# Performance work log

Measured on AMD Instinct MI355X. Metric: run time of the kernel, lower is better.

The kernel has to match this reference:

```python
import jax, jax.numpy as jnp
import numpy as np

# Emformer config (from torchaudio.models.Emformer in BasicNet4)
D, H, FFN, L = 512, 4, 128, 4      # input_dim, num_heads, ffn_dim, num_layers
SEG, RC = 4, 1                     # segment_length, right_context_length
B, T = 8, 1025
U = T - RC                         # utterance length = 1024
NSEG = -(-U // SEG)                # 256 segments
R = NSEG * RC                      # total right-context frames = 256
DH = D // H


def _right_context_indices():
    # torchaudio _gen_right_context: segment i's right context = frames [(i+1)*SEG : (i+1)*SEG+RC],
    # last block = input[T-RC:]
    idx = [np.arange((i + 1) * SEG, (i + 1) * SEG + RC) for i in range(NSEG - 1)]
    idx.append(np.arange(T - RC, T))
    return np.concatenate(idx)


def _attention_mask():
    # Rows / cols ordered [right-context blocks (seg order), utterance frames].
    # A query belonging to segment i may attend to segment i's right-context block
    # and segment i's utterance frames (left_context_length=0, no memory bank).
    seg_rc = np.repeat(np.arange(NSEG), RC)
    seg_u = np.arange(U) // SEG
    seg_q = np.concatenate([seg_rc, seg_u])
    seg_k = np.concatenate([seg_rc, seg_u])
    return seg_q[:, None] == seg_k[None, :]  # (R+U, R+U), True = allowed


def _ln(x, g, b, eps=1e-5):
    mu = jnp.mean(x, -1, keepdims=True)
    var = jnp.mean(jnp.square(x - mu), -1, keepdims=True)
    return (x - mu) * jax.lax.rsqrt(var + eps) * g + b


def setup_inputs() -> dict:
    key = jax.random.key(0)
    ks = jax.random.split(key, 8)
    s = 0.02
    return {
        "x": jax.random.normal(ks[0], (B, T, D), jnp.float32),
        "Wq": jax.random.normal(ks[1], (L, D, D), jnp.float32) * s,
        "bq": jnp.zeros((L, D), jnp.float32),
        "Wkv": jax.random.normal(ks[2], (L, 2 * D, D), jnp.float32) * s,
        "bkv": jnp.zeros((L, 2 * D), jnp.float32),
        "Wo": jax.random.normal(ks[3], (L, D, D), jnp.float32) * s,
        "bo": jnp.zeros((L, D), jnp.float32),
        "W1": jax.random.normal(ks[4], (L, FFN, D), jnp.float32) * s,
        "b1": jnp.zeros((L, FFN), jnp.float32),
        "W2": jax.random.normal(ks[5], (L, D, FFN), jnp.float32) * s,
        "b2": jnp.zeros((L, D), jnp.float32),
        "ln_in_g": jnp.ones((L, D), jnp.float32),
        "ln_in_b": jnp.zeros((L, D), jnp.float32),
        "ff_ln_g": jnp.ones((L, D), jnp.float32),
        "ff_ln_b": jnp.zeros((L, D), jnp.float32),
        "ln_out_g": jnp.ones((L, D), jnp.float32),
        "ln_out_b": jnp.zeros((L, D), jnp.float32),
    }


def reference(x, Wq, bq, Wkv, bkv, Wo, bo, W1, b1, W2, b2,
              ln_in_g, ln_in_b, ff_ln_g, ff_ln_b, ln_out_g, ln_out_b):
    rc_idx = jnp.asarray(_right_context_indices())
    allowed = jnp.asarray(_attention_mask())
    scale = DH ** -0.5
    u = x[:, :U]          # (B, U, D) utterance
    r = x[:, rc_idx]      # (B, R, D) gathered right-context blocks
    for l in range(L):
        cat = jnp.concatenate([r, u], axis=1)            # (B, R+U, D)
        ln = _ln(cat, ln_in_g[l], ln_in_b[l])            # pre-attention LN
        q = (ln @ Wq[l].T + bq[l]).reshape(B, R + U, H, DH)
        kv = ln @ Wkv[l].T + bkv[l]
        k = kv[..., :D].reshape(B, R + U, H, DH)
        v = kv[..., D:].reshape(B, R + U, H, DH)
        scores = jnp.einsum("bqhd,bkhd->bhqk", q * scale, k)
        scores = jnp.where(allowed, scores, -jnp.inf)
        probs = jax.nn.softmax(scores, axis=-1)
        attn = jnp.einsum("bhqk,bkhd->bqhd", probs, v).reshape(B, R + U, D)
        rc_out = attn @ Wo[l].T + bo[l] + cat            # residual w/ pre-LN input
        h = _ln(rc_out, ff_ln_g[l], ff_ln_b[l])
        h = jax.nn.relu(h @ W1[l].T + b1[l]) @ W2[l].T + b2[l]
        rc_out = _ln(rc_out + h, ln_out_g[l], ln_out_b[l])
        r, u = rc_out[:, :R], rc_out[:, R:]
    return u.mean(axis=1)  # (B, D): mean-pool over utterance frames
```

## Files before the change

### kernel.cpp

```cpp
#include <hip/hip_runtime.h>
#include <cstdint>
#include <cstddef>

#define D_    512
#define H_    4
#define DH_   128
#define FFN_  128
#define L_    4
#define B_    8
#define T_    1025
#define U_    1024
#define NSEG_ 256
#define R_    256
#define TOT_  1280
#define M_    (B_*TOT_)
#define CH_   1536

typedef __attribute__((ext_vector_type(8))) short bf16x8;
typedef __attribute__((ext_vector_type(4))) float f32x4;
typedef unsigned short u16;

__device__ __forceinline__ u16 f2bf(float f) {
  unsigned u = __builtin_bit_cast(unsigned, f);
  u += 0x7fff + ((u >> 16) & 1);
  return (u16)(u >> 16);
}
__device__ __forceinline__ float bf2f(u16 h) {
  unsigned u = ((unsigned)h) << 16;
  return __builtin_bit_cast(float, u);
}

__device__ __forceinline__ void gload_lds16(const void* g, void* l) {
  __builtin_amdgcn_global_load_lds(
      (const __attribute__((address_space(1))) unsigned*)g,
      (__attribute__((address_space(3))) unsigned*)l, 16, 0, 0);
}

__global__ __launch_bounds__(256)
void cvt_all_k(const float* __restrict__ Wq, const float* __restrict__ Wkv,
               const float* __restrict__ Wo, const float* __restrict__ W1,
               const float* __restrict__ W2, const float* __restrict__ bq,
               const float* __restrict__ bkv,
               u16* __restrict__ WQKVb, u16* __restrict__ Wob,
               u16* __restrict__ W1b, u16* __restrict__ W2b,
               float* __restrict__ bQKV) {
  int i4 = blockIdx.x * 256 + threadIdx.x;
  if (i4 < 786432) {
    int e = i4 * 4;
    int l = e / 786432;
    int rem = e - l * 786432;
    int n = rem >> 9, k = rem & 511;
    const float* src = (n < 512) ? (Wq + (size_t)l * 262144 + n * 512 + k)
                                 : (Wkv + (size_t)l * 524288 + (n - 512) * 512 + k);
    float4 v = *(const float4*)src;
    ushort4 o; o.x = f2bf(v.x); o.y = f2bf(v.y); o.z = f2bf(v.z); o.w = f2bf(v.w);
    *(ushort4*)(WQKVb + e) = o;
  } else if (i4 < 1048576) {
    int e = (i4 - 786432) * 4;
    float4 v = *(const float4*)(Wo + e);
    ushort4 o; o.x = f2bf(v.x); o.y = f2bf(v.y); o.z = f2bf(v.z); o.w = f2bf(v.w);
    *(ushort4*)(Wob + e) = o;
  } else if (i4 < 1114112) {
    int e = (i4 - 1048576) * 4;
    float4 v = *(const float4*)(W1 + e);
    ushort4 o; o.x = f2bf(v.x); o.y = f2bf(v.y); o.z = f2bf(v.z); o.w = f2bf(v.w);
    *(ushort4*)(W1b + e) = o;
  } else if (i4 < 1179648) {
    int e = (i4 - 1114112) * 4;
    float4 v = *(const float4*)(W2 + e);
    ushort4 o; o.x = f2bf(v.x); o.y = f2bf(v.y); o.z = f2bf(v.z); o.w = f2bf(v.w);
    *(ushort4*)(W2b + e) = o;
  } else if (i4 < 1181184) {
    int e = (i4 - 1179648) * 4;
    int l = e / 1536, n = e - l * 1536;
#pragma unroll
    for (int t = 0; t < 4; ++t) {
      int nn = n + t;
      bQKV[e + t] = (nn < 512) ? bq[l * 512 + nn] : bkv[l * 1024 + (nn - 512)];
    }
  }
}

__global__ __launch_bounds__(256)
void gather_ln_k(const float* __restrict__ x, const float* __restrict__ g,
                 const float* __restrict__ bb, float* __restrict__ X,
                 u16* __restrict__ LNb) {
  int row = blockIdx.x;
  int tid = threadIdx.x;
  int b = row / TOT_, p = row % TOT_;
  int t = (p < R_) ? ((p < R_ - 1) ? 4 * (p + 1) : (T_ - 1)) : (p - R_);
  const float* xr = x + ((size_t)b * T_ + t) * D_;
  float e0 = xr[tid], e1 = xr[tid + 256];
  X[(size_t)row * D_ + tid] = e0;
  X[(size_t)row * D_ + tid + 256] = e1;
  float s = e0 + e1, ss = e0 * e0 + e1 * e1;
#pragma unroll
  for (int off = 32; off > 0; off >>= 1) {
    s  += __shfl_down(s, off);
    ss += __shfl_down(ss, off);
  }
  __shared__ float red[10];
  int wid = tid >> 6, lane = tid & 63;
  if (lane == 0) { red[wid] = s; red[4 + wid] = ss; }
  __syncthreads();
  if (tid == 0) {
    float S = red[0] + red[1] + red[2] + red[3];
    float SS = red[4] + red[5] + red[6] + red[7];
    float mu = S * (1.0f / D_);
    float var = SS * (1.0f / D_) - mu * mu;
    if (var < 0.f) var = 0.f;
    red[8] = mu; red[9] = rsqrtf(var + 1e-5f);
  }
  __syncthreads();
  float mu = red[8], rs = red[9];
  u16* yr = LNb + (size_t)row * D_;
  yr[tid]       = f2bf((e0 - mu) * rs * g[tid]       + bb[tid]);
  yr[tid + 256] = f2bf((e1 - mu) * rs * g[tid + 256] + bb[tid + 256]);
}

#define GBK 32

__global__ __launch_bounds__(256)
void gemm_qkv(const u16* __restrict__ A, const u16* __restrict__ Bw,
              const float* __restrict__ bias, u16* __restrict__ Cout) {
  __shared__ __align__(16) u16 As[128 * GBK];
  __shared__ __align__(16) u16 Bs[128 * GBK];
  const int tid = threadIdx.x;
  const int wid = tid >> 6;
  const int lane = tid & 63;
  const int bid = blockIdx.x;
  const int xcd = bid & 7;
  const int t = bid >> 3;
  const int cb = t % 12;
  const int rb = xcd * 10 + t / 12;
  const int bm = rb * 128;
  const int bn = cb * 128;
  const int wr = wid >> 1, wc = wid & 1;

  const int srow = tid >> 2;
  const int skoff = (tid & 3) << 3;

  f32x4 acc[4][4] = {};

  const u16* Ag0 = A  + (size_t)(bm + srow)      * D_ + skoff;
  const u16* Ag1 = A  + (size_t)(bm + 64 + srow) * D_ + skoff;
  const u16* Bg0 = Bw + (size_t)(bn + srow)      * D_ + skoff;
  const u16* Bg1 = Bw + (size_t)(bn + 64 + srow) * D_ + skoff;
  u16* AsW0 = &As[(size_t)(wid * 16)      * GBK];
  u16* AsW1 = &As[(size_t)(64 + wid * 16) * GBK];
  u16* BsW0 = &Bs[(size_t)(wid * 16)      * GBK];
  u16* BsW1 = &Bs[(size_t)(64 + wid * 16) * GBK];

  const int lrow = lane & 15;
  const int lko  = (lane >> 4) * 16;

  for (int k0 = 0; k0 < D_; k0 += GBK) {
    __syncthreads();
    gload_lds16(Ag0 + k0, AsW0);
    gload_lds16(Ag1 + k0, AsW1);
    gload_lds16(Bg0 + k0, BsW0);
    gload_lds16(Bg1 + k0, BsW1);
    __syncthreads();

    bf16x8 afrag[4], bfrag[4];
#pragma unroll
    for (int m = 0; m < 4; ++m) {
      int row = wr * 64 + m * 16 + lrow;
      afrag[m] = *(const bf16x8*)((const char*)As + row * (GBK * 2) + lko);
    }
#pragma unroll
    for (int n = 0; n < 4; ++n) {
      int col = wc * 64 + n * 16 + lrow;
      bfrag[n] = *(const bf16x8*)((const char*)Bs + col * (GBK * 2) + lko);
    }
#pragma unroll
    for (int m = 0; m < 4; ++m)
#pragma unroll
      for (int n = 0; n < 4; ++n)
        acc[m][n] = __builtin_amdgcn_mfma_f32_16x16x32_bf16(
            afrag[m], bfrag[n], acc[m][n], 0, 0, 0);
  }

  const int lcol  = lane & 15;
  const int lrow4 = (lane >> 4) * 4;
#pragma unroll
  for (int m = 0; m < 4; ++m) {
    int rowbase = bm + wr * 64 + m * 16 + lrow4;
#pragma unroll
    for (int n = 0; n < 4; ++n) {
      int col = bn + wc * 64 + n * 16 + lcol;
      float bv = bias[col];
#pragma unroll
      for (int j = 0; j < 4; ++j) {
        int row = rowbase + j;
        Cout[(size_t)row * CH_ + col] = f2bf(acc[m][n][j] + bv);
      }
    }
  }
}

__global__ __launch_bounds__(256)
void gemm_oproj(const u16* __restrict__ A, const u16* __restrict__ Bw,
                const float* __restrict__ bias, float* __restrict__ Xio) {
  __shared__ __align__(16) u16 As[128 * GBK];
  __shared__ __align__(16) u16 Bs[128 * GBK];
  const int tid = threadIdx.x;
  const int wid = tid >> 6;
  const int lane = tid & 63;
  const int bid = blockIdx.x;
  const int xcd = bid & 7;
  const int t = bid >> 3;
  const int cb = t & 3;
  const int rb = xcd * 10 + (t >> 2);
  const int bm = rb * 128;
  const int bn = cb * 128;
  const int wr = wid >> 1, wc = wid & 1;

  const int srow = tid >> 2;
  const int skoff = (tid & 3) << 3;

  f32x4 acc[4][4] = {};

  const u16* Ag0 = A  + (size_t)(bm + srow)      * D_ + skoff;
  const u16* Ag1 = A  + (size_t)(bm + 64 + srow) * D_ + skoff;
  const u16* Bg0 = Bw + (size_t)(bn + srow)      * D_ + skoff;
  const u16* Bg1 = Bw + (size_t)(bn + 64 + srow) * D_ + skoff;
  u16* AsW0 = &As[(size_t)(wid * 16)      * GBK];
  u16* AsW1 = &As[(size_t)(64 + wid * 16) * GBK];
  u16* BsW0 = &Bs[(size_t)(wid * 16)      * GBK];
  u16* BsW1 = &Bs[(size_t)(64 + wid * 16) * GBK];

  const int lrow = lane & 15;
  const int lko  = (lane >> 4) * 16;

  for (int k0 = 0; k0 < D_; k0 += GBK) {
    __syncthreads();
    gload_lds16(Ag0 + k0, AsW0);
    gload_lds16(Ag1 + k0, AsW1);
    gload_lds16(Bg0 + k0, BsW0);
    gload_lds16(Bg1 + k0, BsW1);
    __syncthreads();

    bf16x8 afrag[4], bfrag[4];
#pragma unroll
    for (int m = 0; m < 4; ++m) {
      int row = wr * 64 + m * 16 + lrow;
      afrag[m] = *(const bf16x8*)((const char*)As + row * (GBK * 2) + lko);
    }
#pragma unroll
    for (int n = 0; n < 4; ++n) {
      int col = wc * 64 + n * 16 + lrow;
      bfrag[n] = *(const bf16x8*)((const char*)Bs + col * (GBK * 2) + lko);
    }
#pragma unroll
    for (int m = 0; m < 4; ++m)
#pragma unroll
      for (int n = 0; n < 4; ++n)
        acc[m][n] = __builtin_amdgcn_mfma_f32_16x16x32_bf16(
            afrag[m], bfrag[n], acc[m][n], 0, 0, 0);
  }

  const int lcol  = lane & 15;
  const int lrow4 = (lane >> 4) * 4;
#pragma unroll
  for (int m = 0; m < 4; ++m) {
    int rowbase = bm + wr * 64 + m * 16 + lrow4;
#pragma unroll
    for (int n = 0; n < 4; ++n) {
      int col = bn + wc * 64 + n * 16 + lcol;
      float bv = bias[col];
#pragma unroll
      for (int j = 0; j < 4; ++j) {
        size_t idx = (size_t)(rowbase + j) * D_ + col;
        Xio[idx] = acc[m][n][j] + bv + Xio[idx];
      }
    }
  }
}

template <int MODE>
__global__ __launch_bounds__(256)
void ffn_fused(const float* __restrict__ X,
               const float* __restrict__ gff, const float* __restrict__ bff,
               const u16* __restrict__ W1, const float* __restrict__ b1,
               const u16* __restrict__ W2, const float* __restrict__ b2,
               const float* __restrict__ g1, const float* __restrict__ b1o,
               const float* __restrict__ g2, const float* __restrict__ b2i,
               float* __restrict__ Xout, u16* __restrict__ OutBf) {
  __shared__ __align__(16) u16 Bs[512 * 32];
  __shared__ __align__(16) u16 Aln[16 * 512];
  __shared__ float wsum[4][16], wss[4][16], mu_s[16], rs_s[16];
  u16* Hs = Aln;
  const int tid = threadIdx.x;
  const int wid = tid >> 6, lane = tid & 63;
  const int bm = blockIdx.x * 16;
  const int r  = tid >> 4;
  const int jj = tid & 15;

  {
    const float* xr = X + (size_t)(bm + r) * D_ + jj * 32;
    float v[32];
    float s = 0.f, ss = 0.f;
#pragma unroll
    for (int i = 0; i < 8; ++i) {
      float4 q = *(const float4*)(xr + i * 4);
      v[i * 4 + 0] = q.x; v[i * 4 + 1] = q.y;
      v[i * 4 + 2] = q.z; v[i * 4 + 3] = q.w;
      s  += q.x + q.y + q.z + q.w;
      ss += q.x * q.x + q.y * q.y + q.z * q.z + q.w * q.w;
    }
#pragma unroll
    for (int off = 1; off < 16; off <<= 1) {
      s  += __shfl_xor(s, off);
      ss += __shfl_xor(ss, off);
    }
    float mu = s * (1.0f / D_);
    float var = ss * (1.0f / D_) - mu * mu;
    if (var < 0.f) var = 0.f;
    float rs = rsqrtf(var + 1e-5f);
    char* Ab = (char*)Aln;
#pragma unroll
    for (int i = 0; i < 8; ++i) {
      int c0 = jj * 32 + i * 4;
      float4 g4 = *(const float4*)(gff + c0);
      float4 b4 = *(const float4*)(bff + c0);
      ushort4 o;
      o.x = f2bf((v[i * 4 + 0] - mu) * rs * g4.x + b4.x);
      o.y = f2bf((v[i * 4 + 1] - mu) * rs * g4.y + b4.y);
      o.z = f2bf((v[i * 4 + 2] - mu) * rs * g4.z + b4.z);
      o.w = f2bf((v[i * 4 + 3] - mu) * rs * g4.w + b4.w);
      int byteoff = (r * 1024 + c0 * 2) ^ ((r & 7) << 4);
      *(ushort4*)(Ab + byteoff) = o;
    }
  }
  __syncthreads();

  const int lrow = lane & 15;
  const int lko  = (lane >> 4) << 4;
  const int l4 = lane >> 2;
  const int k8 = (lane & 3) << 3;
  f32x4 accA[2] = {};

  for (int k0 = 0; k0 < D_; k0 += 32) {
    if (k0) __syncthreads();
#pragma unroll
    for (int p = 0; p < 2; ++p) {
      int rowb = wid * 32 + p * 16 + l4;
      gload_lds16(W1 + (size_t)rowb * D_ + k0 + k8,
                  (char*)Bs + (wid * 32 + p * 16) * 64);
    }
    __syncthreads();
    bf16x8 af = *(const bf16x8*)((const char*)Aln +
                  ((lrow * 1024 + k0 * 2 + lko) ^ ((lrow & 7) << 4)));
    bf16x8 bf[2];
#pragma unroll
    for (int n = 0; n < 2; ++n)
      bf[n] = *(const bf16x8*)((const char*)Bs + (wid * 32 + n * 16 + lrow) * 64 + lko);
#pragma unroll
    for (int n = 0; n < 2; ++n)
      accA[n] = __builtin_amdgcn_mfma_f32_16x16x32_bf16(af, bf[n], accA[n], 0, 0, 0);
  }

  const int lcol = lane & 15;
  const int lr4 = (lane >> 4) * 4;
  __syncthreads();

#pragma unroll
  for (int n = 0; n < 2; ++n) {
    int col = wid * 32 + n * 16 + lcol;
    float bv = b1[col];
#pragma unroll
    for (int j = 0; j < 4; ++j) {
      int rr = lr4 + j;
      float hv = fmaxf(accA[n][j] + bv, 0.f);
      int byteoff = (rr * 256 + col * 2) ^ ((rr & 7) << 4);
      *(u16*)((char*)Hs + byteoff) = f2bf(hv);
    }
  }

  f32x4 acc[8] = {};
  for (int k0 = 0; k0 < FFN_; k0 += 32) {
    __syncthreads();
#pragma unroll
    for (int p = 0; p < 8; ++p) {
      int row = wid * 128 + p * 16 + l4;
      gload_lds16(W2 + (size_t)row * FFN_ + k0 + k8,
                  (char*)Bs + (wid * 128 + p * 16) * 64);
    }
    __syncthreads();

    bf16x8 af = *(const bf16x8*)((const char*)Hs +
                  ((lrow * 256 + k0 * 2 + lko) ^ ((lrow & 7) << 4)));
    bf16x8 bf[8];
#pragma unroll
    for (int n = 0; n < 8; ++n)
      bf[n] = *(const bf16x8*)((const char*)Bs + (wid * 128 + n * 16 + lrow) * 64 + lko);
#pragma unroll
    for (int n = 0; n < 8; ++n)
      acc[n] = __builtin_amdgcn_mfma_f32_16x16x32_bf16(af, bf[n], acc[n], 0, 0, 0);
  }

#pragma unroll
  for (int n = 0; n < 8; ++n) {
    int col = wid * 128 + n * 16 + lcol;
    float bv = b2[col];
#pragma unroll
    for (int j = 0; j < 4; ++j) {
      int row = bm + lr4 + j;
      acc[n][j] = acc[n][j] + bv + X[(size_t)row * D_ + col];
    }
  }

  {
    float s0[4] = {}, s1[4] = {};
#pragma unroll
    for (int n = 0; n < 8; ++n)
#pragma unroll
      for (int j = 0; j < 4; ++j) {
        float v = acc[n][j];
        s0[j] += v; s1[j] += v * v;
      }
#pragma unroll
    for (int off = 1; off < 16; off <<= 1)
#pragma unroll
      for (int j = 0; j < 4; ++j) {
        s0[j] += __shfl_xor(s0[j], off);
        s1[j] += __shfl_xor(s1[j], off);
      }
    if ((lane & 15) == 0) {
#pragma unroll
      for (int j = 0; j < 4; ++j) {
        wsum[wid][lr4 + j] = s0[j]; wss[wid][lr4 + j] = s1[j];
      }
    }
  }
  __syncthreads();
  if (tid < 16) {
    float S  = wsum[0][tid] + wsum[1][tid] + wsum[2][tid] + wsum[3][tid];
    float SS = wss[0][tid] + wss[1][tid] + wss[2][tid] + wss[3][tid];
    float mu = S * (1.0f / D_);
    float var = SS * (1.0f / D_) - mu * mu;
    if (var < 0.f) var = 0.f;
    mu_s[tid] = mu; rs_s[tid] = rsqrtf(var + 1e-5f);
  }
  __syncthreads();

  float gg[8], bv2[8];
#pragma unroll
  for (int n = 0; n < 8; ++n) {
    int col = wid * 128 + n * 16 + lcol;
    gg[n] = g1[col]; bv2[n] = b1o[col];
  }
#pragma unroll
  for (int n = 0; n < 8; ++n) {
    int col = wid * 128 + n * 16 + lcol;
#pragma unroll
    for (int j = 0; j < 4; ++j) {
      int rr = lr4 + j;
      int row = bm + rr;
      float ln = (acc[n][j] - mu_s[rr]) * rs_s[rr] * gg[n] + bv2[n];
      Xout[(size_t)row * D_ + col] = ln;
      acc[n][j] = ln;
    }
  }

  if (MODE == 1) {
    __syncthreads();
    {
      float s0[4] = {}, s1[4] = {};
#pragma unroll
      for (int n = 0; n < 8; ++n)
#pragma unroll
        for (int j = 0; j < 4; ++j) {
          float v = acc[n][j];
          s0[j] += v; s1[j] += v * v;
        }
#pragma unroll
      for (int off = 1; off < 16; off <<= 1)
#pragma unroll
        for (int j = 0; j < 4; ++j) {
          s0[j] += __shfl_xor(s0[j], off);
          s1[j] += __shfl_xor(s1[j], off);
        }
      if ((lane & 15) == 0) {
#pragma unroll
        for (int j = 0; j < 4; ++j) {
          wsum[wid][lr4 + j] = s0[j]; wss[wid][lr4 + j] = s1[j];
        }
      }
    }
    __syncthreads();
    if (tid < 16) {
      float S  = wsum[0][tid] + wsum[1][tid] + wsum[2][tid] + wsum[3][tid];
      float SS = wss[0][tid] + wss[1][tid] + wss[2][tid] + wss[3][tid];
      float mu = S * (1.0f / D_);
      float var = SS * (1.0f / D_) - mu * mu;
      if (var < 0.f) var = 0.f;
      mu_s[tid] = mu; rs_s[tid] = rsqrtf(var + 1e-5f);
    }
    __syncthreads();
#pragma unroll
    for (int n = 0; n < 8; ++n) {
      int col = wid * 128 + n * 16 + lcol;
      gg[n] = g2[col]; bv2[n] = b2i[col];
    }
#pragma unroll
    for (int n = 0; n < 8; ++n) {
      int col = wid * 128 + n * 16 + lcol;
#pragma unroll
      for (int j = 0; j < 4; ++j) {
        int rr = lr4 + j;
        int row = bm + rr;
        float ln = (acc[n][j] - mu_s[rr]) * rs_s[rr] * gg[n] + bv2[n];
        OutBf[(size_t)row * D_ + col] = f2bf(ln);
      }
    }
  }
}

#define QLD 516
__global__ __launch_bounds__(256)
void attn_k(const u16* __restrict__ QKV, u16* __restrict__ O) {
  int bs = blockIdx.x;
  int b = bs >> 8, s = bs & 255;
  __shared__ float Qs[5][QLD];
  __shared__ float Ks[5][QLD];
  __shared__ float Vs[5][QLD];
  __shared__ float P[H_][5][5];
  int tid = threadIdx.x;
  const float scale = 0.08838834764831845f;
  int rows[5];
  rows[0] = s;
#pragma unroll
  for (int i = 1; i < 5; ++i) rows[i] = R_ + 4 * s + (i - 1);
  for (int idx = tid; idx < 960; idx += 256) {
    int mtx = idx / 320;
    int rem = idx - mtx * 320;
    int i = rem >> 6, c8 = rem & 63;
    size_t base = ((size_t)b * TOT_ + rows[i]) * CH_ + mtx * 512 + c8 * 8;
    bf16x8 v = *(const bf16x8*)(QKV + base);
    float* dst = (mtx == 0) ? &Qs[i][c8 * 8] : (mtx == 1 ? &Ks[i][c8 * 8] : &Vs[i][c8 * 8]);
    if (mtx == 0) {
#pragma unroll
      for (int t = 0; t < 8; ++t) dst[t] = bf2f((u16)v[t]) * scale;
    } else {
#pragma unroll
      for (int t = 0; t < 8; ++t) dst[t] = bf2f((u16)v[t]);
    }
  }
  __syncthreads();
  int h = tid >> 6, lane = tid & 63;
  if (lane < 25) {
    int i = lane / 5, j = lane % 5;
    float sum = 0.f;
    const float* qp = &Qs[i][h * DH_];
    const float* kp = &Ks[j][h * DH_];
#pragma unroll 8
    for (int d = 0; d < DH_; ++d) sum += qp[d] * kp[d];
    P[h][i][j] = sum;
  }
  __syncthreads();
  if (lane < 5) {
    int i = lane;
    float m = P[h][i][0];
#pragma unroll
    for (int j = 1; j < 5; ++j) m = fmaxf(m, P[h][i][j]);
    float e[5], ssum = 0.f;
#pragma unroll
    for (int j = 0; j < 5; ++j) { e[j] = __expf(P[h][i][j] - m); ssum += e[j]; }
    float inv = 1.0f / ssum;
#pragma unroll
    for (int j = 0; j < 5; ++j) P[h][i][j] = e[j] * inv;
  }
  __syncthreads();
  for (int idx = lane; idx < 5 * DH_; idx += 64) {
    int i = idx >> 7, d = idx & (DH_ - 1);
    float o = 0.f;
#pragma unroll
    for (int j = 0; j < 5; ++j) o += P[h][i][j] * Vs[j][h * DH_ + d];
    O[((size_t)b * TOT_ + rows[i]) * D_ + h * DH_ + d] = f2bf(o);
  }
}

__global__ __launch_bounds__(256)
void mean_part_k(const float* __restrict__ X, float* __restrict__ part) {
  int d = blockIdx.x * 256 + threadIdx.x;
  int jc = blockIdx.y;
  int b = blockIdx.z;
  float acc = 0.f;
  const float* base = X + ((size_t)b * TOT_ + R_ + jc * 128) * D_ + d;
  for (int j = 0; j < 128; ++j) acc += base[(size_t)j * D_];
  part[((size_t)b * 8 + jc) * D_ + d] = acc;
}

__global__ __launch_bounds__(256)
void mean_final_k(const float* __restrict__ part, float* __restrict__ out) {
  int i = blockIdx.x * 256 + threadIdx.x;
  int b = i >> 9, d = i & (D_ - 1);
  float acc = 0.f;
#pragma unroll
  for (int c = 0; c < 8; ++c) acc += part[((size_t)b * 8 + c) * D_ + d];
  out[i] = acc * (1.0f / U_);
}

extern "C" void kernel_launch(void* const* d_in, const int* in_sizes, int n_in,
                              void* d_out, int out_size, void* d_ws, size_t ws_size,
                              hipStream_t stream) {
  const float* x      = (const float*)d_in[0];
  const float* Wq     = (const float*)d_in[1];
  const float* bq     = (const float*)d_in[2];
  const float* Wkv    = (const float*)d_in[3];
  const float* bkv    = (const float*)d_in[4];
  const float* Wo     = (const float*)d_in[5];
  const float* bo     = (const float*)d_in[6];
  const float* W1     = (const float*)d_in[7];
  const float* b1     = (const float*)d_in[8];
  const float* W2     = (const float*)d_in[9];
  const float* b2     = (const float*)d_in[10];
  const float* ln_in_g  = (const float*)d_in[11];
  const float* ln_in_b  = (const float*)d_in[12];
  const float* ff_ln_g  = (const float*)d_in[13];
  const float* ff_ln_b  = (const float*)d_in[14];
  const float* ln_out_g = (const float*)d_in[15];
  const float* ln_out_b = (const float*)d_in[16];
  float* out = (float*)d_out;

  char* wsb = (char*)d_ws;
  float* X     = (float*)wsb;
  u16*   LNbuf = (u16*)(wsb + 20971520);
  u16*   QKV   = (u16*)(wsb + 31457280);
  u16*   ATT   = (u16*)(wsb + 62914560);
  float* part  = (float*)(wsb + 86507520);
  u16*   WQKVb = (u16*)(wsb + 86638592);
  u16*   Wob   = (u16*)(wsb + 92930048);
  u16*   W1b   = (u16*)(wsb + 95027200);
  u16*   W2b   = (u16*)(wsb + 95551488);
  float* bQKV  = (float*)(wsb + 96075776);

  cvt_all_k<<<4614, 256, 0, stream>>>(Wq, Wkv, Wo, W1, W2, bq, bkv,
                                      WQKVb, Wob, W1b, W2b, bQKV);
  gather_ln_k<<<M_, 256, 0, stream>>>(x, ln_in_g, ln_in_b, X, LNbuf);

  for (int l = 0; l < L_; ++l) {
    const u16* WQKV_l = WQKVb + (size_t)l * CH_ * D_;
    const u16* Wo_l   = Wob   + (size_t)l * D_ * D_;
    const u16* W1_l   = W1b   + (size_t)l * FFN_ * D_;
    const u16* W2_l   = W2b   + (size_t)l * D_ * FFN_;
    const float* bQKV_l = bQKV + (size_t)l * CH_;
    const float* bo_l = bo + (size_t)l * D_;
    const float* b1_l = b1 + (size_t)l * FFN_;
    const float* b2_l = b2 + (size_t)l * D_;

    gemm_qkv<<<960, 256, 0, stream>>>(LNbuf, WQKV_l, bQKV_l, QKV);

    attn_k<<<B_ * NSEG_, 256, 0, stream>>>(QKV, ATT);

    gemm_oproj<<<320, 256, 0, stream>>>(ATT, Wo_l, bo_l, X);

    if (l < L_ - 1) {
      ffn_fused<1><<<M_ / 16, 256, 0, stream>>>(
          X, ff_ln_g + l * D_, ff_ln_b + l * D_,
          W1_l, b1_l, W2_l, b2_l,
          ln_out_g + l * D_, ln_out_b + l * D_,
          ln_in_g + (l + 1) * D_, ln_in_b + (l + 1) * D_,
          X, LNbuf);
    } else {
      ffn_fused<2><<<M_ / 16, 256, 0, stream>>>(
          X, ff_ln_g + l * D_, ff_ln_b + l * D_,
          W1_l, b1_l, W2_l, b2_l,
          ln_out_g + l * D_, ln_out_b + l * D_,
          nullptr, nullptr,
          X, nullptr);
    }
  }

  mean_part_k<<<dim3(2, 8, 8), 256, 0, stream>>>(X, part);
  mean_final_k<<<(B_ * D_) / 256, 256, 0, stream>>>(part, out);
}
```

Measured before the change: 388.2 us.

## Merge setup kernels, fold query scale into weights, bf16 K/V in LDS, single mean kernel

The weight-conversion and gather+LayerNorm kernels are merged into one launch, using block-index ranges to split the work. The attention scale is folded into the bf16 Wq and bq during conversion, so attention no longer multiplies Q. K and V are kept as packed bf16 in LDS instead of being widened to float, which cuts LDS size and store work. The two-stage mean reduction becomes one 16-block kernel, trading one launch for far fewer parallel blocks, each summing 1024 rows serially.

```diff
diff --git a/kernel.cpp b/kernel.cpp
--- a/kernel.cpp
+++ b/kernel.cpp
@@ -36,15 +36,60 @@
       (__attribute__((address_space(3))) unsigned*)l, 16, 0, 0);
 }
 
+#define QSCALE 0.08838834764831845f
+
+#define CVT_BLOCKS 4614
+#define SETUP_GRID (CVT_BLOCKS + M_)
+
 __global__ __launch_bounds__(256)
-void cvt_all_k(const float* __restrict__ Wq, const float* __restrict__ Wkv,
-               const float* __restrict__ Wo, const float* __restrict__ W1,
-               const float* __restrict__ W2, const float* __restrict__ bq,
-               const float* __restrict__ bkv,
-               u16* __restrict__ WQKVb, u16* __restrict__ Wob,
-               u16* __restrict__ W1b, u16* __restrict__ W2b,
-               float* __restrict__ bQKV) {
-  int i4 = blockIdx.x * 256 + threadIdx.x;
+void cvt_gather_k(const float* __restrict__ Wq, const float* __restrict__ Wkv,
+                  const float* __restrict__ Wo, const float* __restrict__ W1,
+                  const float* __restrict__ W2, const float* __restrict__ bq,
+                  const float* __restrict__ bkv,
+                  u16* __restrict__ WQKVb, u16* __restrict__ Wob,
+                  u16* __restrict__ W1b, u16* __restrict__ W2b,
+                  float* __restrict__ bQKV,
+                  const float* __restrict__ x, const float* __restrict__ g,
+                  const float* __restrict__ bb, float* __restrict__ X,
+                  u16* __restrict__ LNb) {
+  __shared__ float red[10];
+  const int bid = blockIdx.x;
+  const int tid = threadIdx.x;
+
+  if (bid >= CVT_BLOCKS) {
+    int row = bid - CVT_BLOCKS;
+    int b = row / TOT_, p = row % TOT_;
+    int t = (p < R_) ? ((p < R_ - 1) ? 4 * (p + 1) : (T_ - 1)) : (p - R_);
+    const float* xr = x + ((size_t)b * T_ + t) * D_;
+    float e0 = xr[tid], e1 = xr[tid + 256];
+    X[(size_t)row * D_ + tid] = e0;
+    X[(size_t)row * D_ + tid + 256] = e1;
+    float s = e0 + e1, ss = e0 * e0 + e1 * e1;
+#pragma unroll
+    for (int off = 32; off > 0; off >>= 1) {
+      s  += __shfl_down(s, off);
+      ss += __shfl_down(ss, off);
+    }
+    int wid = tid >> 6, lane = tid & 63;
+    if (lane == 0) { red[wid] = s; red[4 + wid] = ss; }
+    __syncthreads();
+    if (tid == 0) {
+      float S = red[0] + red[1] + red[2] + red[3];
+      float SS = red[4] + red[5] + red[6] + red[7];
+      float mu = S * (1.0f / D_);
+      float var = SS * (1.0f / D_) - mu * mu;
+      if (var < 0.f) var = 0.f;
+      red[8] = mu; red[9] = rsqrtf(var + 1e-5f);
+    }
+    __syncthreads();
+    float mu = red[8], rs = red[9];
+    u16* yr = LNb + (size_t)row * D_;
+    yr[tid]       = f2bf((e0 - mu) * rs * g[tid]       + bb[tid]);
+    yr[tid + 256] = f2bf((e1 - mu) * rs * g[tid + 256] + bb[tid + 256]);
+    return;
+  }
+
+  int i4 = bid * 256 + tid;
   if (i4 < 786432) {
     int e = i4 * 4;
     int l = e / 786432;
@@ -53,6 +98,7 @@
     const float* src = (n < 512) ? (Wq + (size_t)l * 262144 + n * 512 + k)
                                  : (Wkv + (size_t)l * 524288 + (n - 512) * 512 + k);
     float4 v = *(const float4*)src;
+    if (n < 512) { v.x *= QSCALE; v.y *= QSCALE; v.z *= QSCALE; v.w *= QSCALE; }
     ushort4 o; o.x = f2bf(v.x); o.y = f2bf(v.y); o.z = f2bf(v.z); o.w = f2bf(v.w);
     *(ushort4*)(WQKVb + e) = o;
   } else if (i4 < 1048576) {
@@ -76,46 +122,10 @@
 #pragma unroll
     for (int t = 0; t < 4; ++t) {
       int nn = n + t;
-      bQKV[e + t] = (nn < 512) ? bq[l * 512 + nn] : bkv[l * 1024 + (nn - 512)];
-    }
-  }
-}
-
-__global__ __launch_bounds__(256)
-void gather_ln_k(const float* __restrict__ x, const float* __restrict__ g,
-                 const float* __restrict__ bb, float* __restrict__ X,
-                 u16* __restrict__ LNb) {
-  int row = blockIdx.x;
-  int tid = threadIdx.x;
-  int b = row / TOT_, p = row % TOT_;
-  int t = (p < R_) ? ((p < R_ - 1) ? 4 * (p + 1) : (T_ - 1)) : (p - R_);
-  const float* xr = x + ((size_t)b * T_ + t) * D_;
-  float e0 = xr[tid], e1 = xr[tid + 256];
-  X[(size_t)row * D_ + tid] = e0;
-  X[(size_t)row * D_ + tid + 256] = e1;
-  float s = e0 + e1, ss = e0 * e0 + e1 * e1;
-#pragma unroll
-  for (int off = 32; off > 0; off >>= 1) {
-    s  += __shfl_down(s, off);
-    ss += __shfl_down(ss, off);
-  }
-  __shared__ float red[10];
-  int wid = tid >> 6, lane = tid & 63;
-  if (lane == 0) { red[wid] = s; red[4 + wid] = ss; }
-  __syncthreads();
-  if (tid == 0) {
-    float S = red[0] + red[1] + red[2] + red[3];
-    float SS = red[4] + red[5] + red[6] + red[7];
-    float mu = S * (1.0f / D_);
-    float var = SS * (1.0f / D_) - mu * mu;
-    if (var < 0.f) var = 0.f;
-    red[8] = mu; red[9] = rsqrtf(var + 1e-5f);
-  }
-  __syncthreads();
-  float mu = red[8], rs = red[9];
-  u16* yr = LNb + (size_t)row * D_;
-  yr[tid]       = f2bf((e0 - mu) * rs * g[tid]       + bb[tid]);
-  yr[tid + 256] = f2bf((e1 - mu) * rs * g[tid + 256] + bb[tid + 256]);
+      bQKV[e + t] = (nn < 512) ? bq[l * 512 + nn] * QSCALE
+                               : bkv[l * 1024 + (nn - 512)];
+    }
+  }
 }
 
 #define GBK 32
@@ -519,16 +529,16 @@
 }
 
 #define QLD 516
+#define KLD 528
 __global__ __launch_bounds__(256)
 void attn_k(const u16* __restrict__ QKV, u16* __restrict__ O) {
   int bs = blockIdx.x;
   int b = bs >> 8, s = bs & 255;
   __shared__ float Qs[5][QLD];
-  __shared__ float Ks[5][QLD];
-  __shared__ float Vs[5][QLD];
+  __shared__ __align__(16) u16 Ks[5][KLD];
+  __shared__ __align__(16) u16 Vs[5][KLD];
   __shared__ float P[H_][5][5];
   int tid = threadIdx.x;
-  const float scale = 0.08838834764831845f;
   int rows[5];
   rows[0] = s;
 #pragma unroll
@@ -539,13 +549,14 @@
     int i = rem >> 6, c8 = rem & 63;
     size_t base = ((size_t)b * TOT_ + rows[i]) * CH_ + mtx * 512 + c8 * 8;
     bf16x8 v = *(const bf16x8*)(QKV + base);
-    float* dst = (mtx == 0) ? &Qs[i][c8 * 8] : (mtx == 1 ? &Ks[i][c8 * 8] : &Vs[i][c8 * 8]);
     if (mtx == 0) {
-#pragma unroll
-      for (int t = 0; t < 8; ++t) dst[t] = bf2f((u16)v[t]) * scale;
+      float* dst = &Qs[i][c8 * 8];
+#pragma unroll
+      for (int t = 0; t < 8; ++t) dst[t] = bf2f((u16)v[t]);
+    } else if (mtx == 1) {
+      *(bf16x8*)((char*)&Ks[i][0] + c8 * 16) = v;
     } else {
-#pragma unroll
-      for (int t = 0; t < 8; ++t) dst[t] = bf2f((u16)v[t]);
+      *(bf16x8*)((char*)&Vs[i][0] + c8 * 16) = v;
     }
   }
   __syncthreads();
@@ -554,9 +565,9 @@
     int i = lane / 5, j = lane % 5;
     float sum = 0.f;
     const float* qp = &Qs[i][h * DH_];
-    const float* kp = &Ks[j][h * DH_];
+    const u16* kp = &Ks[j][h * DH_];
 #pragma unroll 8
-    for (int d = 0; d < DH_; ++d) sum += qp[d] * kp[d];
+    for (int d = 0; d < DH_; ++d) sum += qp[d] * bf2f(kp[d]);
     P[h][i][j] = sum;
   }
   __syncthreads();
@@ -577,30 +588,24 @@
     int i = idx >> 7, d = idx & (DH_ - 1);
     float o = 0.f;
 #pragma unroll
-    for (int j = 0; j < 5; ++j) o += P[h][i][j] * Vs[j][h * DH_ + d];
+    for (int j = 0; j < 5; ++j) o += P[h][i][j] * bf2f(Vs[j][h * DH_ + d]);
     O[((size_t)b * TOT_ + rows[i]) * D_ + h * DH_ + d] = f2bf(o);
   }
 }
 
 __global__ __launch_bounds__(256)
-void mean_part_k(const float* __restrict__ X, float* __restrict__ part) {
-  int d = blockIdx.x * 256 + threadIdx.x;
-  int jc = blockIdx.y;
-  int b = blockIdx.z;
-  float acc = 0.f;
-  const float* base = X + ((size_t)b * TOT_ + R_ + jc * 128) * D_ + d;
-  for (int j = 0; j < 128; ++j) acc += base[(size_t)j * D_];
-  part[((size_t)b * 8 + jc) * D_ + d] = acc;
-}
-
-__global__ __launch_bounds__(256)
-void mean_final_k(const float* __restrict__ part, float* __restrict__ out) {
-  int i = blockIdx.x * 256 + threadIdx.x;
-  int b = i >> 9, d = i & (D_ - 1);
-  float acc = 0.f;
-#pragma unroll
-  for (int c = 0; c < 8; ++c) acc += part[((size_t)b * 8 + c) * D_ + d];
-  out[i] = acc * (1.0f / U_);
+void mean_k(const float* __restrict__ X, float* __restrict__ out) {
+  int b = blockIdx.x >> 1;
+  int d = (blockIdx.x & 1) * 256 + threadIdx.x;
+  const float* base = X + ((size_t)b * TOT_ + R_) * D_ + d;
+  float a0 = 0.f, a1 = 0.f, a2 = 0.f, a3 = 0.f;
+  for (int j = 0; j < U_; j += 4) {
+    a0 += base[(size_t)(j + 0) * D_];
+    a1 += base[(size_t)(j + 1) * D_];
+    a2 += base[(size_t)(j + 2) * D_];
+    a3 += base[(size_t)(j + 3) * D_];
+  }
+  out[b * D_ + d] = (a0 + a1 + a2 + a3) * (1.0f / U_);
 }
 
 extern "C" void kernel_launch(void* const* d_in, const int* in_sizes, int n_in,
@@ -630,16 +635,15 @@
   u16*   LNbuf = (u16*)(wsb + 20971520);
   u16*   QKV   = (u16*)(wsb + 31457280);
   u16*   ATT   = (u16*)(wsb + 62914560);
-  float* part  = (float*)(wsb + 86507520);
   u16*   WQKVb = (u16*)(wsb + 86638592);
   u16*   Wob   = (u16*)(wsb + 92930048);
   u16*   W1b   = (u16*)(wsb + 95027200);
   u16*   W2b   = (u16*)(wsb + 95551488);
   float* bQKV  = (float*)(wsb + 96075776);
 
-  cvt_all_k<<<4614, 256, 0, stream>>>(Wq, Wkv, Wo, W1, W2, bq, bkv,
-                                      WQKVb, Wob, W1b, W2b, bQKV);
-  gather_ln_k<<<M_, 256, 0, stream>>>(x, ln_in_g, ln_in_b, X, LNbuf);
+  cvt_gather_k<<<SETUP_GRID, 256, 0, stream>>>(Wq, Wkv, Wo, W1, W2, bq, bkv,
+                                               WQKVb, Wob, W1b, W2b, bQKV,
+                                               x, ln_in_g, ln_in_b, X, LNbuf);
 
   for (int l = 0; l < L_; ++l) {
     const u16* WQKV_l = WQKVb + (size_t)l * CH_ * D_;
@@ -674,6 +678,5 @@
     }
   }
 
-  mean_part_k<<<dim3(2, 8, 8), 256, 0, stream>>>(X, part);
-  mean_final_k<<<(B_ * D_) / 256, 256, 0, stream>>>(part, out);
-}
+  mean_k<<<16, 256, 0, stream>>>(X, out);
+}
```

Measured after the change: 409.0 us. 1.05x slower.
